# Kernel tuning notes

Measured on AMD Instinct MI355X. Metric: run time of the kernel, lower is better.

Reference implementation:

```python
import jax, jax.numpy as jnp
import numpy as np
import math

B, T, D = 1, 4096, 1024
H = 16
HD = D // H  # 64


def _rotate_half(x):
    d = x.shape[-1] // 2
    return jnp.concatenate([-x[..., d:], x[..., :d]], axis=-1)


def setup_inputs() -> dict:
    key = jax.random.key(0)
    k1, k2, k3 = jax.random.split(key, 3)
    x = jax.random.normal(k1, (B, T, D), dtype=jnp.float32)
    # Linear weights stored as (in, out) so forward is x @ W
    w_qkv = jax.random.normal(k2, (D, 3 * D), dtype=jnp.float32) * (1.0 / math.sqrt(D))
    w_proj = jax.random.normal(k3, (D, D), dtype=jnp.float32) * (1.0 / math.sqrt(D))
    return {"x": x, "w_qkv": w_qkv, "w_proj": w_proj}


def reference(x, w_qkv, w_proj):
    b, t, c = x.shape
    qkv = x @ w_qkv  # [b,t,3c]
    q, k, v = jnp.split(qkv, 3, axis=-1)
    # [b,h,t,hd]
    q = q.reshape(b, t, H, HD).transpose(0, 2, 1, 3)
    k = k.reshape(b, t, H, HD).transpose(0, 2, 1, 3)
    v = v.reshape(b, t, H, HD).transpose(0, 2, 1, 3)

    # RoPE (rotate_half style)
    inv_freq = 1.0 / (10000.0 ** (jnp.arange(0, HD, 2, dtype=jnp.float32) / HD))
    pos = jnp.arange(t, dtype=jnp.float32)
    freqs = jnp.outer(pos, inv_freq)            # [t, hd/2]
    cos = jnp.concatenate([jnp.cos(freqs), jnp.cos(freqs)], axis=-1)[None, None]  # [1,1,t,hd]
    sin = jnp.concatenate([jnp.sin(freqs), jnp.sin(freqs)], axis=-1)[None, None]
    q = q * cos + _rotate_half(q) * sin
    k = k * cos + _rotate_half(k) * sin

    att = jnp.einsum('bhqd,bhkd->bhqk', q, k) / math.sqrt(HD)  # [b,h,t,t]
    causal = jnp.tril(jnp.ones((t, t), dtype=bool))
    att = jnp.where(causal, att, -jnp.inf)
    att = jax.nn.softmax(att, axis=-1)
    # dropout is identity in eval mode
    y = jnp.einsum('bhqk,bhkd->bhqd', att, v)
    y = y.transpose(0, 2, 1, 3).reshape(b, t, c)
    return y @ w_proj
```

## Files before the change

kernel.cpp:

```cpp
#include <hip/hip_runtime.h>
#include <hip/hip_fp16.h>
#include <math.h>

#define TT 4096
#define DD 1024
#define NH 16
#define HD 64

typedef __attribute__((ext_vector_type(8))) _Float16 half8v;
typedef __attribute__((ext_vector_type(4))) _Float16 half4v;
typedef __attribute__((ext_vector_type(4))) float f32x4;

#define GLDS16(g, l)                                                        \
    __builtin_amdgcn_global_load_lds(                                       \
        (const __attribute__((address_space(1))) void*)(g),                 \
        (__attribute__((address_space(3))) void*)(l), 16, 0, 0)

__global__ __launch_bounds__(256) void cast_x(const float* __restrict__ X,
                                              _Float16* __restrict__ Xh)
{
    const int i = (blockIdx.x * 256 + threadIdx.x) * 8;
    float4 a = *(const float4*)&X[i];
    float4 b = *(const float4*)&X[i + 4];
    half8v o = {(_Float16)a.x, (_Float16)a.y, (_Float16)a.z, (_Float16)a.w,
                (_Float16)b.x, (_Float16)b.y, (_Float16)b.z, (_Float16)b.w};
    *(half8v*)&Xh[i] = o;
}

__global__ __launch_bounds__(256) void transpose_cast(
    const float* __restrict__ W, _Float16* __restrict__ WT, int K, int N)
{
    __shared__ float tile[64][65];
    const int t = threadIdx.x;
    const int k0 = blockIdx.y * 64, n0 = blockIdx.x * 64;
    const int c = (t & 15) * 4, r = t >> 4;
#pragma unroll
    for (int i = 0; i < 4; i++) {
        float4 v = *(const float4*)&W[(size_t)(k0 + r + 16 * i) * N + n0 + c];
        tile[r + 16 * i][c + 0] = v.x;
        tile[r + 16 * i][c + 1] = v.y;
        tile[r + 16 * i][c + 2] = v.z;
        tile[r + 16 * i][c + 3] = v.w;
    }
    __syncthreads();
#pragma unroll
    for (int i = 0; i < 4; i++) {
        const int n = r + 16 * i;
        half4v o;
        o[0] = (_Float16)tile[c + 0][n];
        o[1] = (_Float16)tile[c + 1][n];
        o[2] = (_Float16)tile[c + 2][n];
        o[3] = (_Float16)tile[c + 3][n];
        *(half4v*)&WT[(size_t)(n0 + n) * K + k0 + c] = o;
    }
}

template <int MODE>
__global__ __launch_bounds__(256) void gemm_h(
    const _Float16* __restrict__ A, const _Float16* __restrict__ Bt,
    float* __restrict__ C0, _Float16* __restrict__ Q,
    _Float16* __restrict__ Kk, _Float16* __restrict__ V,
    int M, int N, int K)
{
    __shared__ _Float16 As[128 * 32];
    __shared__ _Float16 Bs[128 * 32];
    const int tid  = threadIdx.x;
    const int wave = tid >> 6;
    const int lane = tid & 63;
    const int quad = lane >> 4;
    const int n16  = lane & 15;
    const int n0 = blockIdx.x * 128;
    const int m0 = blockIdx.y * 128;
    const int wr = (wave & 1) * 64;
    const int wc = (wave >> 1) * 64;

    f32x4 acc[4][4];
#pragma unroll
    for (int i = 0; i < 4; i++)
#pragma unroll
        for (int j = 0; j < 4; j++) acc[i][j] = (f32x4){0.f, 0.f, 0.f, 0.f};

    const int srow = tid >> 2;
    const int scol = (tid & 3) * 8;
    const _Float16* Ag = A + (size_t)(m0 + srow) * K + scol;
    const _Float16* Bg = Bt + (size_t)(n0 + srow) * K + scol;
    _Float16* AsW = As + (size_t)wave * 512;
    _Float16* BsW = Bs + (size_t)wave * 512;

    for (int k0 = 0; k0 < K; k0 += 32) {
        __syncthreads();
        GLDS16(Ag + k0, AsW);
        GLDS16(Ag + (size_t)64 * K + k0, AsW + 2048);
        GLDS16(Bg + k0, BsW);
        GLDS16(Bg + (size_t)64 * K + k0, BsW + 2048);
        __syncthreads();

        half8v aF[4], bF[4];
#pragma unroll
        for (int i = 0; i < 4; i++)
            aF[i] = *(const half8v*)&As[(size_t)(wr + i * 16 + n16) * 32 + quad * 8];
#pragma unroll
        for (int j = 0; j < 4; j++)
            bF[j] = *(const half8v*)&Bs[(size_t)(wc + j * 16 + n16) * 32 + quad * 8];
#pragma unroll
        for (int i = 0; i < 4; i++)
#pragma unroll
            for (int j = 0; j < 4; j++)
                acc[i][j] = __builtin_amdgcn_mfma_f32_16x16x32_f16(
                    aF[i], bF[j], acc[i][j], 0, 0, 0);
    }

    if (MODE == 0) {
#pragma unroll
        for (int i = 0; i < 4; i++)
#pragma unroll
            for (int j = 0; j < 4; j++)
#pragma unroll
                for (int r = 0; r < 4; r++) {
                    const int m = m0 + wr + i * 16 + quad * 4 + r;
                    const int n = n0 + wc + j * 16 + n16;
                    C0[(size_t)m * N + n] = acc[i][j][r];
                }
    } else {
        const int ncol0 = n0 + wc;
        const int which = ncol0 >> 10;
        const int h = (ncol0 & 1023) >> 6;
        if (which < 2) {
            _Float16* dst = (which == 0) ? Q : Kk;
            const float sc = (which == 0) ? 0.125f * 1.44269504f : 1.0f;
            const float K2 = 0.4152410118609203f;
#pragma unroll
            for (int jlo = 0; jlo < 2; jlo++) {
                const int d = jlo * 16 + n16;
                const float invf = exp2f(-(float)d * K2);
#pragma unroll
                for (int i = 0; i < 4; i++) {
#pragma unroll
                    for (int r = 0; r < 4; r++) {
                        const int t = m0 + wr + i * 16 + quad * 4 + r;
                        const float f = (float)t * invf;
                        float sn, cs;
                        __sincosf(f, &sn, &cs);
                        const float lo = acc[i][jlo][r];
                        const float hi = acc[i][jlo + 2][r];
                        const size_t off = ((size_t)h * TT + t) * HD + d;
                        dst[off]      = (_Float16)((lo * cs - hi * sn) * sc);
                        dst[off + 32] = (_Float16)((hi * cs + lo * sn) * sc);
                    }
                }
            }
        } else {
#pragma unroll
            for (int i = 0; i < 4; i++)
#pragma unroll
                for (int j = 0; j < 4; j++)
#pragma unroll
                    for (int r = 0; r < 4; r++) {
                        const int t = m0 + wr + i * 16 + quad * 4 + r;
                        const int d = j * 16 + n16;
                        const int cp = 2 * (t & 15) + ((t >> 4) & 1);
                        V[(((size_t)h * (TT / 32) + (t >> 5)) * 64 + d) * 32 + cp] =
                            (_Float16)acc[i][j][r];
                    }
        }
    }
}

__global__ __launch_bounds__(256) void zero_acc(float4* __restrict__ O4,
                                                float4* __restrict__ L4)
{
    const int i = blockIdx.x * 256 + threadIdx.x;
    const float4 z = {0.f, 0.f, 0.f, 0.f};
    O4[i] = z;
    if (i < 16384) L4[i] = z;
}

__global__ __launch_bounds__(256) void attn_kernel(
    const _Float16* __restrict__ Qh, const _Float16* __restrict__ Kh,
    const _Float16* __restrict__ Vp, _Float16* __restrict__ Oacc,
    float* __restrict__ Lacc)
{
    __shared__ _Float16 Ks[2][32][32];
    __shared__ _Float16 Vs[64][32];
    __shared__ _Float16 Ps[4][32][40];

    const int tid  = threadIdx.x;
    const int wave = tid >> 6;
    const int lane = tid & 63;
    const int quad = lane >> 4;
    const int n16  = lane & 15;
    const int h  = blockIdx.z;
    const int qt = 31 - blockIdx.y;
    const int s  = blockIdx.x;
    const int nT = 4 * qt + 4;
    const int nS = (qt + 4) >> 2;
    if (s >= nS) return;
    const int t_beg = s * nT / nS;
    const int t_end = (s + 1) * nT / nS;

    const int q0 = qt * 128;
    const int rowbase = q0 + wave * 32;

    const _Float16* Qg = Qh + (size_t)h * TT * HD;
    const _Float16* Kg = Kh + (size_t)h * TT * HD;
    const _Float16* Vg = Vp + (size_t)h * (TT / 32) * 2048;

    half8v aQ[2][2];
#pragma unroll
    for (int g = 0; g < 2; g++) {
        const int row = rowbase + g * 16 + n16;
#pragma unroll
        for (int c = 0; c < 2; c++)
            aQ[g][c] = *(const half8v*)(Qg + (size_t)row * HD + c * 32 + quad * 8);
    }

    f32x4 O[2][4], Ol[2];
#pragma unroll
    for (int g = 0; g < 2; g++) {
#pragma unroll
        for (int d = 0; d < 4; d++) O[g][d] = (f32x4){0.f, 0.f, 0.f, 0.f};
        Ol[g] = (f32x4){0.f, 0.f, 0.f, 0.f};
    }
    const half8v vOnes = {(_Float16)1, (_Float16)1, (_Float16)1, (_Float16)1,
                          (_Float16)1, (_Float16)1, (_Float16)1, (_Float16)1};

    const int kc = tid >> 7, kj = (tid >> 2) & 31, ks = tid & 3;
    const _Float16* kSrc = Kg + (size_t)kj * HD + kc * 32 + ks * 8;
    const _Float16* vSrc = Vg + (size_t)tid * 8;
    _Float16* ksBase = &Ks[0][0][0] + (size_t)wave * 512;
    _Float16* vsBase = &Vs[0][0] + (size_t)wave * 512;

    for (int it = t_beg; it < t_end; ++it) {
        const int j0 = it * 32;
        __syncthreads();
        GLDS16(kSrc + (size_t)j0 * HD, ksBase);
        GLDS16(vSrc + (size_t)it * 2048, vsBase);
        __syncthreads();

        if (j0 <= rowbase + 31) {
            const bool needMask = (j0 + 31 > rowbase);

            f32x4 S[2][2];
#pragma unroll
            for (int g = 0; g < 2; g++)
#pragma unroll
                for (int st = 0; st < 2; st++) {
                    S[g][st] = (f32x4){0.f, 0.f, 0.f, 0.f};
#pragma unroll
                    for (int c = 0; c < 2; c++) {
                        half8v bK = *(const half8v*)&Ks[c][st * 16 + n16][quad * 8];
                        S[g][st] = __builtin_amdgcn_mfma_f32_16x16x32_f16(
                            aQ[g][c], bK, S[g][st], 0, 0, 0);
                    }
                }

#pragma unroll
            for (int g = 0; g < 2; g++)
#pragma unroll
                for (int r = 0; r < 4; r++) {
                    const int row = rowbase + g * 16 + quad * 4 + r;
                    float x0 = S[g][0][r];
                    float x1 = S[g][1][r];
                    if (needMask) {
                        x0 = (j0 + n16      <= row) ? x0 : -1e30f;
                        x1 = (j0 + 16 + n16 <= row) ? x1 : -1e30f;
                    }
                    const float p0 = __builtin_amdgcn_exp2f(x0);
                    const float p1 = __builtin_amdgcn_exp2f(x1);
                    *(__half2*)&Ps[wave][g * 16 + quad * 4 + r][2 * n16] =
                        __floats2half2_rn(p0, p1);
                }

            half8v bV[4];
#pragma unroll
            for (int d = 0; d < 4; d++)
                bV[d] = *(const half8v*)&Vs[d * 16 + n16][quad * 8];
#pragma unroll
            for (int g = 0; g < 2; g++) {
                half8v aP = *(const half8v*)&Ps[wave][g * 16 + n16][quad * 8];
#pragma unroll
                for (int d = 0; d < 4; d++)
                    O[g][d] = __builtin_amdgcn_mfma_f32_16x16x32_f16(
                        aP, bV[d], O[g][d], 0, 0, 0);
                Ol[g] = __builtin_amdgcn_mfma_f32_16x16x32_f16(
                    aP, vOnes, Ol[g], 0, 0, 0);
            }
        }
    }

#pragma unroll
    for (int g = 0; g < 2; g++)
#pragma unroll
        for (int r = 0; r < 4; r++) {
            const int row = rowbase + g * 16 + quad * 4 + r;
            if (n16 == 0)
                unsafeAtomicAdd(&Lacc[h * TT + row], Ol[g][r]);
#pragma unroll
            for (int d = 0; d < 4; d++) {
                float v = O[g][d][r];
                float vn = __shfl_xor(v, 1);
                if ((lane & 1) == 0) {
                    __half2* dst = (__half2*)(Oacc +
                        ((size_t)h * TT + row) * HD + d * 16 + n16);
                    unsafeAtomicAdd(dst, __floats2half2_rn(v, vn));
                }
            }
        }
}

__global__ __launch_bounds__(256) void finalize(
    const _Float16* __restrict__ Oacc, const float* __restrict__ Lacc,
    _Float16* __restrict__ Y)
{
    const int gid = blockIdx.x * 256 + threadIdx.x;
    const int h = gid >> 15;
    const int rem = gid & 32767;
    const int t = rem >> 3;
    const int c = rem & 7;
    const float inv = 1.0f / Lacc[h * TT + t];
    half8v o = *(const half8v*)(Oacc + ((size_t)h * TT + t) * HD + c * 8);
    half8v y;
#pragma unroll
    for (int e = 0; e < 8; e++) y[e] = (_Float16)((float)o[e] * inv);
    *(half8v*)(Y + (size_t)t * DD + h * HD + c * 8) = y;
}

extern "C" void kernel_launch(void* const* d_in, const int* in_sizes, int n_in,
                              void* d_out, int out_size, void* d_ws, size_t ws_size,
                              hipStream_t stream)
{
    const float* x      = (const float*)d_in[0];
    const float* w_qkv  = (const float*)d_in[1];
    const float* w_proj = (const float*)d_in[2];
    float* out = (float*)d_out;

    char* ws = (char*)d_ws;
    const size_t MB = 1u << 20;
    _Float16* xh   = (_Float16*)(ws);
    _Float16* WqT  = (_Float16*)(ws + 8 * MB);
    _Float16* WpT  = (_Float16*)(ws + 14 * MB);
    _Float16* Qh   = (_Float16*)(ws + 16 * MB);
    _Float16* Kh   = (_Float16*)(ws + 24 * MB);
    _Float16* Vp   = (_Float16*)(ws + 32 * MB);
    _Float16* Yh   = (_Float16*)(ws + 40 * MB);
    _Float16* Oacc = (_Float16*)(ws + 48 * MB);
    float*    Lacc = (float*)(ws + 57 * MB);

    dim3 blk(256);

    cast_x<<<(TT * DD) / (256 * 8), blk, 0, stream>>>(x, xh);
    transpose_cast<<<dim3(3072 / 64, DD / 64), blk, 0, stream>>>(w_qkv, WqT, DD, 3 * DD);
    transpose_cast<<<dim3(DD / 64, DD / 64), blk, 0, stream>>>(w_proj, WpT, DD, DD);

    gemm_h<1><<<dim3(3072 / 128, TT / 128), blk, 0, stream>>>(
        xh, WqT, nullptr, Qh, Kh, Vp, TT, 3 * DD, DD);

    zero_acc<<<2048, blk, 0, stream>>>((float4*)Oacc, (float4*)Lacc);

    attn_kernel<<<dim3(8, 32, NH), blk, 0, stream>>>(Qh, Kh, Vp, Oacc, Lacc);

    finalize<<<2048, blk, 0, stream>>>(Oacc, Lacc, Yh);

    gemm_h<0><<<dim3(DD / 128, TT / 128), blk, 0, stream>>>(
        Yh, WpT, out, nullptr, nullptr, nullptr, TT, DD, DD);
}
```

Before: 280.7 us.

## Double-buffer 64-key K/V tiles in LDS with swizzled layout and prefetch

The attention kernel now stages K and V in 64-key tiles, up from 32, into two LDS buffers. The next tile is prefetched with global_load_lds while the current tile is computed, so there is one barrier per iteration instead of two. LDS chunk indices get an XOR swizzle to cut bank conflicts on the fragment reads, and the split of the key range across blocks is halved to match the larger tile. This raises LDS use and register pressure (more S and bK fragments). It also depends on the compiler's wait counts letting the prefetch actually overlap the compute.

```diff
diff --git a/kernel.cpp b/kernel.cpp
--- a/kernel.cpp
+++ b/kernel.cpp
@@ -180,8 +180,8 @@
     const _Float16* __restrict__ Vp, _Float16* __restrict__ Oacc,
     float* __restrict__ Lacc)
 {
-    __shared__ _Float16 Ks[2][32][32];
-    __shared__ _Float16 Vs[64][32];
+    __shared__ _Float16 Ks[2][2][64][32];
+    __shared__ _Float16 Vs[2][2][64][32];
     __shared__ _Float16 Ps[4][32][40];
 
     const int tid  = threadIdx.x;
@@ -192,7 +192,7 @@
     const int h  = blockIdx.z;
     const int qt = 31 - blockIdx.y;
     const int s  = blockIdx.x;
-    const int nT = 4 * qt + 4;
+    const int nT = 2 * qt + 2;
     const int nS = (qt + 4) >> 2;
     if (s >= nS) return;
     const int t_beg = s * nT / nS;
@@ -224,46 +224,71 @@
     const half8v vOnes = {(_Float16)1, (_Float16)1, (_Float16)1, (_Float16)1,
                           (_Float16)1, (_Float16)1, (_Float16)1, (_Float16)1};
 
-    const int kc = tid >> 7, kj = (tid >> 2) & 31, ks = tid & 3;
-    const _Float16* kSrc = Kg + (size_t)kj * HD + kc * 32 + ks * 8;
-    const _Float16* vSrc = Vg + (size_t)tid * 8;
-    _Float16* ksBase = &Ks[0][0][0] + (size_t)wave * 512;
-    _Float16* vsBase = &Vs[0][0] + (size_t)wave * 512;
+    const int srow = tid >> 2;
+    const int schk = tid & 3;
+    const int sswz = schk ^ ((srow >> 1) & 3);
+    const _Float16* kSrc = Kg + (size_t)srow * HD + sswz * 8;
+    const _Float16* vSrc = Vg + (size_t)srow * 32 + sswz * 8;
+    _Float16* ksB0 = &Ks[0][0][0][0] + (size_t)wave * 512;
+    _Float16* vsB0 = &Vs[0][0][0][0] + (size_t)wave * 512;
+
+    const int slot = (quad ^ ((n16 >> 1) & 3)) * 8;
+
+#define STAGE(buf, it)                                                        \
+    do {                                                                      \
+        const size_t ko = (size_t)(it) * 64 * HD;                             \
+        GLDS16(kSrc + ko,      ksB0 + (size_t)(buf) * 4096);                  \
+        GLDS16(kSrc + ko + 32, ksB0 + (size_t)(buf) * 4096 + 2048);           \
+        const size_t vo = (size_t)(it) * 4096;                                \
+        GLDS16(vSrc + vo,        vsB0 + (size_t)(buf) * 4096);                \
+        GLDS16(vSrc + vo + 2048, vsB0 + (size_t)(buf) * 4096 + 2048);         \
+    } while (0)
+
+    STAGE(t_beg & 1, t_beg);
 
     for (int it = t_beg; it < t_end; ++it) {
-        const int j0 = it * 32;
+        const int j0 = it * 64;
         __syncthreads();
-        GLDS16(kSrc + (size_t)j0 * HD, ksBase);
-        GLDS16(vSrc + (size_t)it * 2048, vsBase);
-        __syncthreads();
-
-        if (j0 <= rowbase + 31) {
-            const bool needMask = (j0 + 31 > rowbase);
-
-            f32x4 S[2][2];
-#pragma unroll
-            for (int g = 0; g < 2; g++)
-#pragma unroll
-                for (int st = 0; st < 2; st++) {
-                    S[g][st] = (f32x4){0.f, 0.f, 0.f, 0.f};
-#pragma unroll
-                    for (int c = 0; c < 2; c++) {
-                        half8v bK = *(const half8v*)&Ks[c][st * 16 + n16][quad * 8];
-                        S[g][st] = __builtin_amdgcn_mfma_f32_16x16x32_f16(
-                            aQ[g][c], bK, S[g][st], 0, 0, 0);
-                    }
-                }
+        if (it + 1 < t_end) STAGE((it + 1) & 1, it + 1);
+        const int b = it & 1;
+
+        if (j0 > rowbase + 31) continue;
+
+        half8v bK[2][4];
+#pragma unroll
+        for (int c = 0; c < 2; c++)
+#pragma unroll
+            for (int st = 0; st < 4; st++)
+                bK[c][st] = *(const half8v*)&Ks[b][c][st * 16 + n16][slot];
+
+        f32x4 S[2][4];
+#pragma unroll
+        for (int g = 0; g < 2; g++)
+#pragma unroll
+            for (int st = 0; st < 4; st++) {
+                S[g][st] = (f32x4){0.f, 0.f, 0.f, 0.f};
+#pragma unroll
+                for (int c = 0; c < 2; c++)
+                    S[g][st] = __builtin_amdgcn_mfma_f32_16x16x32_f16(
+                        aQ[g][c], bK[c][st], S[g][st], 0, 0, 0);
+            }
+
+#pragma unroll
+        for (int hv = 0; hv < 2; hv++) {
+            const int jh = j0 + hv * 32;
+            if (jh > rowbase + 31) continue;
+            const bool needMask = (jh + 31 > rowbase);
 
 #pragma unroll
             for (int g = 0; g < 2; g++)
 #pragma unroll
                 for (int r = 0; r < 4; r++) {
                     const int row = rowbase + g * 16 + quad * 4 + r;
-                    float x0 = S[g][0][r];
-                    float x1 = S[g][1][r];
+                    float x0 = S[g][2 * hv][r];
+                    float x1 = S[g][2 * hv + 1][r];
                     if (needMask) {
-                        x0 = (j0 + n16      <= row) ? x0 : -1e30f;
-                        x1 = (j0 + 16 + n16 <= row) ? x1 : -1e30f;
+                        x0 = (jh + n16      <= row) ? x0 : -1e30f;
+                        x1 = (jh + 16 + n16 <= row) ? x1 : -1e30f;
                     }
                     const float p0 = __builtin_amdgcn_exp2f(x0);
                     const float p1 = __builtin_amdgcn_exp2f(x1);
@@ -274,7 +299,7 @@
             half8v bV[4];
 #pragma unroll
             for (int d = 0; d < 4; d++)
-                bV[d] = *(const half8v*)&Vs[d * 16 + n16][quad * 8];
+                bV[d] = *(const half8v*)&Vs[b][hv][d * 16 + n16][slot];
 #pragma unroll
             for (int g = 0; g < 2; g++) {
                 half8v aP = *(const half8v*)&Ps[wave][g * 16 + n16][quad * 8];
```

Measured after the change: 307.0 us. 1.09x slower.
